# Optimization experiments

Hardware: AMD Instinct MI355X
Metric: run time of the kernel (lower is better)

Reference implementation:

```python
import jax, jax.numpy as jnp
import numpy as np

IM = 128          # imSize
LEAKY_SLOPE = 0.2 # LeakyReLU(0.2) in embed

# FFT / IFFT modules in the original repo (models/fft_utils.py) are
# torch.fft(x, 2, normalized=True) / torch.ifft(x, 2, normalized=True)
# on (N,H,W,2) re/im pairs -> orthonormal 2D (i)FFT of the complex image.

def _forward(x, mask, conv_w):
    # x: (bz, C, H, W); channels 0,1 = real/imag, channels 2: = 'others'
    bz, C, H, W = x.shape
    img = x[:, 0] + 1j * x[:, 1]                      # (bz, H, W) complex
    kspace = jnp.fft.fft2(img, norm='ortho')          # FFT module
    # seperate_mask keeps only k-space row i in copy i -> one-hot over H.
    eye = jnp.eye(IM, dtype=kspace.dtype)             # (IM, H)
    masked = kspace[:, None, :, :] * eye[None, :, :, None]   # (bz, IM, H, W)
    # batched 2D IFFT of each single-row k-space, then magnitude (norm over re/im)
    sep = jnp.abs(jnp.fft.ifft2(masked, norm='ortho')).astype(x.dtype)  # (bz, IM, H, W)
    # embed: 1x1 conv (IM->IM channels, no bias) + LeakyReLU(0.2)
    emb = jnp.einsum('oc,bchw->bohw', conv_w, sep)
    emb = jnp.where(emb >= 0, emb, LEAKY_SLOPE * emb)
    if C > 2:
        return jnp.concatenate([emb, x[:, 2:]], axis=1)  # (bz, IM + C-2, H, W)
    return emb


def setup_inputs() -> dict:
    key = jax.random.key(0)
    k1, k2, k3 = jax.random.split(key, 3)
    x = jax.random.normal(k1, (8, 3, IM, IM), dtype=jnp.float32)
    mask = jax.random.uniform(k2, (8, 1, IM, IM), dtype=jnp.float32)  # unused by forward (API fidelity)
    conv_w = jax.random.normal(k3, (IM, IM), dtype=jnp.float32) / np.sqrt(IM)
    return {"x": x, "mask": mask, "conv_w": conv_w}


def reference(x, mask, conv_w):
    return _forward(x, mask, conv_w)
```

## Files before the change

### kernel.cpp

```cpp
#include <hip/hip_runtime.h>
#include <math.h>

#define IM 128

__global__ void dft_mag_kernel(const float* __restrict__ x, float* __restrict__ mag) {
    const int blk = blockIdx.x;
    const int b   = blk >> 7;
    const int col = blk & 127;
    const int i   = threadIdx.x;

    __shared__ float re_s[IM], im_s[IM], twc[IM], tws[IM];

    const float* xr = x + (size_t)(b * 3 + 0) * IM * IM;
    const float* xi = x + (size_t)(b * 3 + 1) * IM * IM;
    re_s[i] = xr[i * IM + col];
    im_s[i] = xi[i * IM + col];
    const float ang = (float)(2.0 * M_PI / IM) * (float)i;
    twc[i] = cosf(ang);
    tws[i] = sinf(ang);
    __syncthreads();

    float ar = 0.f, ai = 0.f;
    #pragma unroll 8
    for (int y = 0; y < IM; ++y) {
        const int k  = (i * y) & 127;
        const float c = twc[k];
        const float s = tws[k];
        const float r = re_s[y];
        const float m = im_s[y];
        ar = fmaf(r, c, fmaf(m, s, ar));
        ai = fmaf(m, c, fmaf(-r, s, ai));
    }
    mag[((size_t)b * IM + i) * IM + col] = sqrtf(fmaf(ar, ar, ai * ai)) * (1.0f / IM);
}

__global__ void conv_lrelu_kernel(const float* __restrict__ mag,
                                  const float* __restrict__ cw,
                                  float* __restrict__ E) {
    const int blk = blockIdx.x;
    const int b = blk >> 7;
    const int o = blk & 127;
    const int w = threadIdx.x;
    const float* magb = mag + (size_t)b * IM * IM;
    const float* cwo  = cw + (size_t)o * IM;
    float acc = 0.f;
    #pragma unroll 8
    for (int i = 0; i < IM; ++i) {
        acc = fmaf(cwo[i], magb[i * IM + w], acc);
    }
    acc = acc >= 0.f ? acc : 0.2f * acc;
    E[((size_t)b * IM + o) * IM + w] = acc;
}

__global__ void bcast_kernel(const float4* __restrict__ E4,
                             const float4* __restrict__ x4,
                             float4* __restrict__ out4,
                             int total) {
    const int idx = blockIdx.x * blockDim.x + threadIdx.x;
    if (idx >= total) return;
    const int w4   = idx & 31;
    const int h    = (idx >> 5) & 127;
    const int rest = idx >> 12;
    const int o    = rest % 129;
    const int b    = rest / 129;
    float4 v;
    if (o < 128) {
        v = E4[(size_t)(b * 128 + o) * 32 + w4];
    } else {
        v = x4[((size_t)(b * 3 + 2) * 128 + h) * 32 + w4];
    }
    out4[idx] = v;
}

extern "C" void kernel_launch(void* const* d_in, const int* in_sizes, int n_in,
                              void* d_out, int out_size, void* d_ws, size_t ws_size,
                              hipStream_t stream) {
    const float* x  = (const float*)d_in[0];
    const float* cw = (const float*)d_in[2];
    float* out = (float*)d_out;

    float* mag = (float*)d_ws;
    float* E   = mag + 8 * IM * IM;

    dft_mag_kernel<<<8 * IM, IM, 0, stream>>>(x, mag);
    conv_lrelu_kernel<<<8 * IM, IM, 0, stream>>>(mag, cw, E);

    const int total_f4 = out_size / 4;
    bcast_kernel<<<(total_f4 + 255) / 256, 256, 0, stream>>>(
        (const float4*)E, (const float4*)x, (float4*)out, total_f4);
}
```

Baseline: 33.17 us.

## Fuse column DFT magnitude with 1x1 conv and use recurrence twiddles

Merges the DFT-magnitude kernel and the conv+LeakyReLU kernel into one kernel per (batch, column), so the magnitude column stays in shared memory instead of making a global round trip. The shared-memory twiddle lookup is replaced by a sincos rotation recurrence carried in registers. The conv now reads weight rows as float4 per thread. The recurrence accumulates float rounding error over 128 steps, and the weight reads are strided across threads, which could hurt coalescing.

After: 30.03 us. -9.5%, faster.

```diff
diff --git a/kernel.cpp b/kernel.cpp
--- a/kernel.cpp
+++ b/kernel.cpp
@@ -3,53 +3,58 @@
 
 #define IM 128
 
-__global__ void dft_mag_kernel(const float* __restrict__ x, float* __restrict__ mag) {
+__global__ __launch_bounds__(IM) void dft_conv_kernel(const float* __restrict__ x,
+                                                      const float* __restrict__ cw,
+                                                      float* __restrict__ E) {
     const int blk = blockIdx.x;
     const int b   = blk >> 7;
     const int col = blk & 127;
-    const int i   = threadIdx.x;
+    const int tid = threadIdx.x;
 
-    __shared__ float re_s[IM], im_s[IM], twc[IM], tws[IM];
+    __shared__ float2 data_s[IM];
+    __shared__ float  mag_s[IM];
 
     const float* xr = x + (size_t)(b * 3 + 0) * IM * IM;
     const float* xi = x + (size_t)(b * 3 + 1) * IM * IM;
-    re_s[i] = xr[i * IM + col];
-    im_s[i] = xi[i * IM + col];
-    const float ang = (float)(2.0 * M_PI / IM) * (float)i;
-    twc[i] = cosf(ang);
-    tws[i] = sinf(ang);
+    float2 d;
+    d.x = xr[tid * IM + col];
+    d.y = xi[tid * IM + col];
+    data_s[tid] = d;
+
+    const float ang = (float)(2.0 * M_PI / IM) * (float)tid;
+    float sn, cb;
+    __sincosf(ang, &sn, &cb);
+    const float sb = -sn;
+
     __syncthreads();
 
-    float ar = 0.f, ai = 0.f;
+    float c = 1.f, s = 0.f, ar = 0.f, ai = 0.f;
     #pragma unroll 8
     for (int y = 0; y < IM; ++y) {
-        const int k  = (i * y) & 127;
-        const float c = twc[k];
-        const float s = tws[k];
-        const float r = re_s[y];
-        const float m = im_s[y];
-        ar = fmaf(r, c, fmaf(m, s, ar));
-        ai = fmaf(m, c, fmaf(-r, s, ai));
+        const float2 v = data_s[y];
+        ar = fmaf(v.x, c, fmaf(-v.y, s, ar));
+        ai = fmaf(v.y, c, fmaf( v.x, s, ai));
+        const float t0 = s * sb;
+        const float t1 = c * sb;
+        c = fmaf(c, cb, -t0);
+        s = fmaf(s, cb,  t1);
     }
-    mag[((size_t)b * IM + i) * IM + col] = sqrtf(fmaf(ar, ar, ai * ai)) * (1.0f / IM);
-}
+    mag_s[tid] = sqrtf(fmaf(ar, ar, ai * ai)) * (1.0f / IM);
 
-__global__ void conv_lrelu_kernel(const float* __restrict__ mag,
-                                  const float* __restrict__ cw,
-                                  float* __restrict__ E) {
-    const int blk = blockIdx.x;
-    const int b = blk >> 7;
-    const int o = blk & 127;
-    const int w = threadIdx.x;
-    const float* magb = mag + (size_t)b * IM * IM;
-    const float* cwo  = cw + (size_t)o * IM;
+    __syncthreads();
+
+    const float4* cwo = (const float4*)(cw + (size_t)tid * IM);
     float acc = 0.f;
     #pragma unroll 8
-    for (int i = 0; i < IM; ++i) {
-        acc = fmaf(cwo[i], magb[i * IM + w], acc);
+    for (int g = 0; g < IM / 4; ++g) {
+        const float4 wv = cwo[g];
+        acc = fmaf(wv.x, mag_s[4 * g + 0], acc);
+        acc = fmaf(wv.y, mag_s[4 * g + 1], acc);
+        acc = fmaf(wv.z, mag_s[4 * g + 2], acc);
+        acc = fmaf(wv.w, mag_s[4 * g + 3], acc);
     }
     acc = acc >= 0.f ? acc : 0.2f * acc;
-    E[((size_t)b * IM + o) * IM + w] = acc;
+    E[((size_t)b * IM + tid) * IM + col] = acc;
 }
 
 __global__ void bcast_kernel(const float4* __restrict__ E4,
@@ -79,11 +84,9 @@
     const float* cw = (const float*)d_in[2];
     float* out = (float*)d_out;
 
-    float* mag = (float*)d_ws;
-    float* E   = mag + 8 * IM * IM;
+    float* E = (float*)d_ws;
 
-    dft_mag_kernel<<<8 * IM, IM, 0, stream>>>(x, mag);
-    conv_lrelu_kernel<<<8 * IM, IM, 0, stream>>>(mag, cw, E);
+    dft_conv_kernel<<<8 * IM, IM, 0, stream>>>(x, cw, E);
 
     const int total_f4 = out_size / 4;
     bcast_kernel<<<(total_f4 + 255) / 256, 256, 0, stream>>>(
```
